# Kernel optimization log

Measured on AMD Instinct MI355X. Metric: run time of the kernel, lower is better.

The kernel has to match this reference:

```python
import jax, jax.numpy as jnp
import numpy as np

IGNORE_INDEX = -100
W_HARD = 0.5
W_SOFT = 0.5
TEMPERATURE = 1.0
BETA = 0.0  # forward KL branch
NORMALIZE_TOPK = True


def setup_inputs() -> dict:
    key = jax.random.key(0)
    ks = jax.random.split(key, 6)
    B, N, D, V, K = 2, 2048, 2048, 32768, 64
    student_input = jax.random.normal(ks[0], (B, N, D), dtype=jnp.float32)
    # scale weight so logits are O(1)-ish and logsumexp is well-behaved in fp32
    student_lm_head_weight = jax.random.normal(ks[1], (V, D), dtype=jnp.float32) * 0.02
    target_token_ids = jax.random.randint(ks[2], (B, N, K), 0, V, dtype=jnp.int64)
    # realistic teacher top-k logprobs: normalized over k
    target_logprobs = jax.nn.log_softmax(jax.random.normal(ks[3], (B, N, K), dtype=jnp.float32), axis=-1)
    target_mask = jax.random.randint(ks[4], (B, N, K), 0, 2, dtype=jnp.int32)
    true_labels = jax.random.randint(ks[5], (B, N), 0, V, dtype=jnp.int64)
    return {
        "student_input": student_input,
        "student_lm_head_weight": student_lm_head_weight,
        "target_token_ids": target_token_ids,
        "target_logprobs": target_logprobs,
        "target_mask": target_mask,
        "true_labels": true_labels,
    }


def reference(student_input, student_lm_head_weight, target_token_ids, target_logprobs, target_mask, true_labels):
    B, N, D = student_input.shape
    K = target_token_ids.shape[-1]
    M = B * N

    x = student_input.reshape(M, D)
    logits = x @ student_lm_head_weight.T  # (M, V)

    # ---- hard CE loss on next-token-shifted labels (sum reduction, ignore_index) ----
    labels = jnp.pad(true_labels, ((0, 0), (0, 1)), constant_values=IGNORE_INDEX)[:, 1:].reshape(M)
    lse_full = jax.nn.logsumexp(logits, axis=-1)  # (M,)
    valid = labels != IGNORE_INDEX
    safe_labels = jnp.where(valid, labels, 0)
    gold = jnp.take_along_axis(logits, safe_labels[:, None], axis=-1)[:, 0]
    ce_loss = jnp.sum(jnp.where(valid, lse_full - gold, 0.0))

    # ---- soft top-k forward-KL loss (beta == 0.0) ----
    s_logits = logits / TEMPERATURE
    s_lse = jax.nn.logsumexp(s_logits, axis=-1, keepdims=True)  # (M, 1)
    tk_ids = target_token_ids.reshape(M, K)
    s_lp_topk = jnp.take_along_axis(s_logits, tk_ids, axis=-1) - s_lse  # (M, K)
    if NORMALIZE_TOPK:
        s_lp_topk = jax.nn.log_softmax(s_lp_topk, axis=-1)
    t_lp = target_logprobs.reshape(M, K)
    mask = target_mask.reshape(M, K).astype(bool)
    fwd_kl = jnp.exp(t_lp) * (t_lp - s_lp_topk)  # per-token forward KL terms
    kd_loss = jnp.sum(jnp.where(mask, fwd_kl, 0.0))
    kd_loss = kd_loss * (TEMPERATURE ** 2)

    return W_SOFT * kd_loss + W_HARD * ce_loss
```

## Files before the change

### kernel.cpp

```cpp
#include <hip/hip_runtime.h>
#include <hip/hip_bf16.h>
#include <stdint.h>

typedef __attribute__((ext_vector_type(4))) float f32x4;

#define D_DIM 2048
#define V_DIM 32768
#define M_DIM 4096
#define N_SEQ 2048
#define K_TOP 64
#define NSLOT 512
#define EBCAP 512
#define WSCALE 64.0f
#define IWSCALE 0.015625f

static __device__ __forceinline__ unsigned int f32_to_e4m3(float x) {
  float ax = fminf(fabsf(x), 448.0f);
  unsigned int s = (__float_as_uint(x) >> 31) << 7;
  if (ax >= 0.015625f) {
    unsigned int m = __float_as_uint(ax);
    unsigned int keep = m >> 20;
    unsigned int rb = (m >> 19) & 1u, st = (m & 0x7FFFFu) != 0u;
    keep += rb & (st | (keep & 1u));
    int v = (int)keep - (120 << 3);
    if (v > 0x7E) v = 0x7E;
    return s | (unsigned int)v;
  } else {
    int m = __float2int_rn(ax * 512.0f);
    return s | (unsigned int)m;
  }
}

typedef __attribute__((address_space(3))) unsigned int lds_u32_t;
typedef const __attribute__((address_space(1))) unsigned int glb_u32_t;
static __device__ __forceinline__ void gload16(const void* g, void* l) {
  __builtin_amdgcn_global_load_lds((glb_u32_t*)g, (lds_u32_t*)l, 16, 0, 0);
}

__global__ void cast_fp8_kernel(const float4* __restrict__ inA, uint2* __restrict__ outA, int nA8,
                                const float4* __restrict__ inB, uint2* __restrict__ outB, int nB8) {
  int i = blockIdx.x * blockDim.x + threadIdx.x;
  int stride = gridDim.x * blockDim.x;
  int tot = nA8 + nB8;
  for (; i < tot; i += stride) {
    const float4* in = (i < nA8) ? inA : inB;
    uint2* out = (i < nA8) ? outA : outB;
    float sc = (i < nA8) ? WSCALE : 1.0f;
    int j = (i < nA8) ? i : i - nA8;
    float4 a = in[2 * j], b = in[2 * j + 1];
    uint2 r;
    r.x = f32_to_e4m3(a.x * sc) | (f32_to_e4m3(a.y * sc) << 8) |
          (f32_to_e4m3(a.z * sc) << 16) | (f32_to_e4m3(a.w * sc) << 24);
    r.y = f32_to_e4m3(b.x * sc) | (f32_to_e4m3(b.y * sc) << 8) |
          (f32_to_e4m3(b.z * sc) << 16) | (f32_to_e4m3(b.w * sc) << 24);
    out[j] = r;
  }
}

__global__ __launch_bounds__(256) void bin_kernel(
    const int* __restrict__ tids, const int* __restrict__ tlab,
    unsigned int* __restrict__ cnt, unsigned int* __restrict__ ebuf) {
  int idx = blockIdx.x * 256 + threadIdx.x;
  if (idx >= M_DIM * (K_TOP + 1)) return;
  int m = idx / (K_TOP + 1), k = idx - m * (K_TOP + 1);
  int id;
  if (k < K_TOP) id = tids[m * K_TOP + k];
  else {
    int n = m & (N_SEQ - 1);
    if (n == N_SEQ - 1) return;
    id = tlab[m + 1];
  }
  int tile = ((m >> 8) << 7) + (id >> 8);
  unsigned int pos = atomicAdd(&cnt[tile], 1u);
  if (pos < EBCAP)
    ebuf[tile * EBCAP + pos] =
        ((unsigned int)k << 16) | ((unsigned int)(m & 255) << 8) | (unsigned int)(id & 255);
}


#define BAR do { __builtin_amdgcn_s_barrier(); asm volatile("" ::: "memory"); } while (0)
#define VMC(N) asm volatile("s_waitcnt vmcnt(" #N ")" ::: "memory")
#define PRIO1 __builtin_amdgcn_s_setprio(1)
#define PRIO0 __builtin_amdgcn_s_setprio(0)

#define LD8(BASE, R, KS) \
  (*(const long*)((BASE) + (R) * 64 + \
     (((2 * (KS) + (kqg >> 1)) ^ ((R) & 3) ^ (((R) >> 2) & 3)) << 4) + ((kqg & 1) << 3)))
#define LDA8(BASE, MI, KS) LD8(BASE, (MI) * 16 + fr, KS)
#define LDB8(BASE, NI, KS) LD8(BASE, brow + (NI) * 16 + fr, KS)

#define STAGE(H) do { \
  int tt_ = (H) >> 2, pos_ = (H) & 3; \
  char* dst_ = ldst + ((tt_ & 1) << 15) + (pos_ << 13); \
  const unsigned char* src_ = ((pos_ & 2) ? aptr : bptr) \
      + ((pos_ & 1) ? (size_t)128 * D_DIM : (size_t)0) + (size_t)tt_ * 64; \
  gload16(src_, dst_); \
} while (0)

#define MFMA_Q(M0, U) do { \
  _Pragma("unroll") \
  for (int ni = 0; ni < 4; ++ni) \
    acc[M0][ni] = __builtin_amdgcn_mfma_f32_16x16x32_fp8_fp8(U[0][0], bfrag[ni][0], acc[M0][ni], 0, 0, 0); \
  _Pragma("unroll") \
  for (int ni = 0; ni < 4; ++ni) \
    acc[(M0) + 1][ni] = __builtin_amdgcn_mfma_f32_16x16x32_fp8_fp8(U[1][0], bfrag[ni][0], acc[(M0) + 1][ni], 0, 0, 0); \
  _Pragma("unroll") \
  for (int ni = 0; ni < 4; ++ni) \
    acc[M0][ni] = __builtin_amdgcn_mfma_f32_16x16x32_fp8_fp8(U[0][1], bfrag[ni][1], acc[M0][ni], 0, 0, 0); \
  _Pragma("unroll") \
  for (int ni = 0; ni < 4; ++ni) \
    acc[(M0) + 1][ni] = __builtin_amdgcn_mfma_f32_16x16x32_fp8_fp8(U[1][1], bfrag[ni][1], acc[(M0) + 1][ni], 0, 0, 0); \
} while (0)

#define TILE1B(T, DOST, NVM, DONEXT) do { \
  char* curA_ = ldsAroot + (((T) & 1) << 15); \
  char* nxtA_ = ldsAroot + ((((T) + 1) & 1) << 15); \
  char* nxtB_ = ldsBroot + ((((T) + 1) & 1) << 15); \
   \
  BAR; \
  if (DOST) STAGE(4 * (T) + 8); \
  PRIO1; MFMA_Q(0, aq); PRIO0; \
  aqn[0][0] = LDA8(curA_, 2, 0); aqn[0][1] = LDA8(curA_, 2, 1); \
  aqn[1][0] = LDA8(curA_, 3, 0); aqn[1][1] = LDA8(curA_, 3, 1); \
   \
  BAR; \
  if (DOST) STAGE(4 * (T) + 9); \
  PRIO1; MFMA_Q(2, aqn); PRIO0; \
  aq[0][0] = LDA8(curA_, 4, 0); aq[0][1] = LDA8(curA_, 4, 1); \
  aq[1][0] = LDA8(curA_, 5, 0); aq[1][1] = LDA8(curA_, 5, 1); \
   \
  BAR; \
  PRIO1; MFMA_Q(4, aq); PRIO0; \
  aqn[0][0] = LDA8(curA_, 6, 0); aqn[0][1] = LDA8(curA_, 6, 1); \
  aqn[1][0] = LDA8(curA_, 7, 0); aqn[1][1] = LDA8(curA_, 7, 1); \
  if ((NVM) == 2) { VMC(2); } else if ((NVM) == 0) { VMC(0); } \
   \
  BAR; \
  if (DOST) { STAGE(4 * (T) + 10); STAGE(4 * (T) + 11); } \
  PRIO1; MFMA_Q(6, aqn); PRIO0; \
  if (DONEXT) { \
    _Pragma("unroll") \
    for (int ni = 0; ni < 4; ++ni) { \
      bfrag[ni][0] = LDB8(nxtB_, ni, 0); bfrag[ni][1] = LDB8(nxtB_, ni, 1); } \
    aq[0][0] = LDA8(nxtA_, 0, 0); aq[0][1] = LDA8(nxtA_, 0, 1); \
    aq[1][0] = LDA8(nxtA_, 1, 0); aq[1][1] = LDA8(nxtA_, 1, 1); \
  } \
} while (0)

__global__ __launch_bounds__(512, 2) void gemm_lse_kernel(
    const unsigned char* __restrict__ x8,
    const unsigned char* __restrict__ w8,
    float* __restrict__ pMax,
    float* __restrict__ pSum,
    const unsigned int* __restrict__ bcnt,
    const unsigned int* __restrict__ ebuf,
    float* __restrict__ gout) {
  __shared__ __align__(16) char lds[131072];

  const int bid0 = blockIdx.x;
  const int mt = (bid0 >> 4) & 15;
  const int vt = ((bid0 >> 8) << 4) | (bid0 & 15);
  const int tid = threadIdx.x, lane = tid & 63, w = tid >> 6;
  const int wr = w >> 2, wc = w & 3;
  const int fr = lane & 15, kqg = lane >> 4;
  const int brow = (wc & 1) * 64;

  const int gcol = (((tid & 3) ^ ((tid >> 2) & 3) ^ ((tid >> 4) & 3)) << 4);
  const unsigned char* aptr = x8 + (size_t)(mt * 256 + (tid >> 2)) * D_DIM + gcol;
  const unsigned char* bptr = w8 + (size_t)(vt * 256 + (tid >> 2)) * D_DIM + gcol;
  char* ldst = lds + tid * 16;

  char* ldsAroot = lds + ((2 + wr) << 13);
  char* ldsBroot = lds + ((wc >> 1) << 13);

  f32x4 acc[8][4];
#pragma unroll
  for (int i = 0; i < 8; i++)
#pragma unroll
    for (int j = 0; j < 4; j++) acc[i][j] = (f32x4){0.f, 0.f, 0.f, 0.f};

  long bfrag[4][2], aq[2][2], aqn[2][2];

  STAGE(0); STAGE(1); STAGE(2); STAGE(3);
  STAGE(4); STAGE(5); STAGE(6); STAGE(7);
  VMC(0);
  BAR;
#pragma unroll
  for (int ni = 0; ni < 4; ++ni) {
    bfrag[ni][0] = LDB8(ldsBroot, ni, 0); bfrag[ni][1] = LDB8(ldsBroot, ni, 1);
  }
  aq[0][0] = LDA8(ldsAroot, 0, 0); aq[0][1] = LDA8(ldsAroot, 0, 1);
  aq[1][0] = LDA8(ldsAroot, 1, 0); aq[1][1] = LDA8(ldsAroot, 1, 1);

  for (int it = 0; it < 15; ++it) {
    TILE1B(2 * it, 1, 2, 1);
    TILE1B(2 * it + 1, 1, 2, 1);
  }
  TILE1B(30, 0, 0, 1);
  TILE1B(31, 0, 99, 0);

  const int slot = vt * 4 + wc;
#pragma unroll
  for (int mi = 0; mi < 8; mi++) {
#pragma unroll
    for (int j = 0; j < 4; j++) {
      const int row = mt * 256 + wr * 128 + mi * 16 + kqg * 4 + j;
      float v0 = acc[mi][0][j] * IWSCALE, v1 = acc[mi][1][j] * IWSCALE;
      float v2 = acc[mi][2][j] * IWSCALE, v3 = acc[mi][3][j] * IWSCALE;
      float mx = fmaxf(fmaxf(v0, v1), fmaxf(v2, v3));
      for (int s = 1; s < 16; s <<= 1) mx = fmaxf(mx, __shfl_xor(mx, s));
      float sm = __expf(v0 - mx) + __expf(v1 - mx) +
                 __expf(v2 - mx) + __expf(v3 - mx);
      for (int s = 1; s < 16; s <<= 1) sm += __shfl_xor(sm, s);
      if (fr == 0) {
        pMax[row * NSLOT + slot] = mx;
        pSum[row * NSLOT + slot] = sm;
      }
    }
  }

  const int tile = (mt << 7) + vt;
  unsigned int cn = bcnt[tile];
  if (cn > EBCAP) cn = EBCAP;
  const unsigned int* elist = ebuf + tile * EBCAP;
  float* ldsf = (float*)lds;

  __syncthreads();
#pragma unroll
  for (int half = 0; half < 2; ++half) {
    if (wr == half) {
#pragma unroll
      for (int mi = 0; mi < 8; mi++) {
        const int r0 = mi * 16 + kqg * 4;
        const int cs = (kqg & 1) << 4;
#pragma unroll
        for (int ni = 0; ni < 4; ni++) {
          const int c0 = (wc * 64 + ni * 16 + fr) ^ cs;
#pragma unroll
          for (int j = 0; j < 4; j++)
            ldsf[(r0 + j) * 256 + c0] = acc[mi][ni][j] * IWSCALE;
        }
      }
    }
    __syncthreads();
    for (unsigned int e = tid; e < cn; e += 512) {
      unsigned int u = elist[e];
      int r = (u >> 8) & 255;
      if ((r >> 7) == half) {
        int c = u & 255, k = u >> 16;
        int rl = r & 127;
        gout[(mt * 256 + r) * (K_TOP + 1) + k] = ldsf[rl * 256 + (c ^ (((rl >> 2) & 1) << 4))];
      }
    }
    __syncthreads();
  }
}

__global__ __launch_bounds__(256) void reduce_kernel(
    const float* __restrict__ pMax, const float* __restrict__ pSum,
    const float* __restrict__ gout, const float* __restrict__ t_lp,
    const int* __restrict__ t_mask, float* __restrict__ out) {
  const int tid = threadIdx.x, lane = tid & 63, w = tid >> 6;
  const int m = blockIdx.x * 4 + w;

  float msl[8], ssl[8];
  float M = -1e30f;
#pragma unroll
  for (int j = 0; j < 8; j++) {
    msl[j] = pMax[m * NSLOT + lane + j * 64];
    ssl[j] = pSum[m * NSLOT + lane + j * 64];
    M = fmaxf(M, msl[j]);
  }
  for (int s = 1; s < 64; s <<= 1) M = fmaxf(M, __shfl_xor(M, s));
  float S = 0.f;
#pragma unroll
  for (int j = 0; j < 8; j++) S += ssl[j] * __expf(msl[j] - M);
  for (int s = 1; s < 64; s <<= 1) S += __shfl_xor(S, s);
  const float lse = M + logf(S);

  const int n = m & (N_SEQ - 1);
  float ce = 0.f;
  if (n < N_SEQ - 1) ce = lse - gout[m * (K_TOP + 1) + K_TOP];

  const float g = gout[m * (K_TOP + 1) + lane];
  float gM = g;
  for (int s = 1; s < 64; s <<= 1) gM = fmaxf(gM, __shfl_xor(gM, s));
  float gE = __expf(g - gM);
  float gS = gE;
  for (int s = 1; s < 64; s <<= 1) gS += __shfl_xor(gS, s);
  const float lseK = gM + logf(gS);

  const float tl = t_lp[m * K_TOP + lane];
  const int mk = t_mask[m * K_TOP + lane];
  float kd = mk ? __expf(tl) * (tl - (g - lseK)) : 0.f;
  for (int s = 1; s < 64; s <<= 1) kd += __shfl_xor(kd, s);

  if (lane == 0) atomicAdd(out, 0.5f * kd + 0.5f * ce);
}

extern "C" void kernel_launch(void* const* d_in, const int* in_sizes, int n_in,
                              void* d_out, int out_size, void* d_ws, size_t ws_size,
                              hipStream_t stream) {
  const float* x   = (const float*)d_in[0];
  const float* Wm  = (const float*)d_in[1];
  const int* tids  = (const int*)d_in[2];
  const float* tlp = (const float*)d_in[3];
  const int* tmask = (const int*)d_in[4];
  const int* tlab  = (const int*)d_in[5];
  float* out = (float*)d_out;

  char* ws = (char*)d_ws;
  unsigned char* w8 = (unsigned char*)ws;
  unsigned char* x8 = (unsigned char*)(ws + (size_t)V_DIM * D_DIM);
  char* p = ws + (size_t)V_DIM * D_DIM + (size_t)M_DIM * D_DIM;
  float* pMax = (float*)p;                       p += (size_t)M_DIM * NSLOT * 4;
  float* pSum = (float*)p;                       p += (size_t)M_DIM * NSLOT * 4;
  float* gout = (float*)p;                       p += (size_t)M_DIM * (K_TOP + 1) * 4;
  unsigned int* bcnt = (unsigned int*)p;         p += 2048 * 4;
  unsigned int* ebuf = (unsigned int*)p;         p += (size_t)2048 * EBCAP * 4;

  hipMemsetAsync(d_out, 0, sizeof(float), stream);
  hipMemsetAsync(bcnt, 0, 2048 * 4, stream);

  bin_kernel<<<(M_DIM * (K_TOP + 1) + 255) / 256, 256, 0, stream>>>(
      tids, tlab, bcnt, ebuf);

  cast_fp8_kernel<<<8192, 256, 0, stream>>>(
      (const float4*)Wm, (uint2*)w8, (V_DIM * D_DIM) / 8,
      (const float4*)x, (uint2*)x8, (M_DIM * D_DIM) / 8);

  gemm_lse_kernel<<<(M_DIM / 256) * (V_DIM / 256), 512, 0, stream>>>(
      x8, w8, pMax, pSum, bcnt, ebuf, gout);

  reduce_kernel<<<M_DIM / 4, 256, 0, stream>>>(pMax, pSum, gout, tlp, tmask, out);
}
```

Measured before the change: 570.2 us.

## Permute fp8 K layout so each lane fetches both MFMA fragments with one 16B LDS read

```diff
diff --git a/kernel.cpp b/kernel.cpp
--- a/kernel.cpp
+++ b/kernel.cpp
@@ -3,6 +3,7 @@
 #include <stdint.h>
 
 typedef __attribute__((ext_vector_type(4))) float f32x4;
+typedef __attribute__((ext_vector_type(2))) long l8x16;
 
 #define D_DIM 2048
 #define V_DIM 32768
@@ -53,7 +54,8 @@
           (f32_to_e4m3(a.z * sc) << 16) | (f32_to_e4m3(a.w * sc) << 24);
     r.y = f32_to_e4m3(b.x * sc) | (f32_to_e4m3(b.y * sc) << 8) |
           (f32_to_e4m3(b.z * sc) << 16) | (f32_to_e4m3(b.w * sc) << 24);
-    out[j] = r;
+    int oj = ((j >> 3) << 3) + ((j & 3) << 1) + ((j >> 2) & 1);
+    out[oj] = r;
   }
 }
 
@@ -83,11 +85,10 @@
 #define PRIO1 __builtin_amdgcn_s_setprio(1)
 #define PRIO0 __builtin_amdgcn_s_setprio(0)
 
-#define LD8(BASE, R, KS) \
-  (*(const long*)((BASE) + (R) * 64 + \
-     (((2 * (KS) + (kqg >> 1)) ^ ((R) & 3) ^ (((R) >> 2) & 3)) << 4) + ((kqg & 1) << 3)))
-#define LDA8(BASE, MI, KS) LD8(BASE, (MI) * 16 + fr, KS)
-#define LDB8(BASE, NI, KS) LD8(BASE, brow + (NI) * 16 + fr, KS)
+#define LDF(BASE, R) \
+  (*(const l8x16*)((BASE) + (R) * 64 + ((kqg ^ (((R) >> 1) & 3)) << 4)))
+#define LDAF(BASE, MI) LDF(BASE, (MI) * 16 + fr)
+#define LDBF(BASE, NI) LDF(BASE, brow + (NI) * 16 + fr)
 
 #define STAGE(H) do { \
   int tt_ = (H) >> 2, pos_ = (H) & 3; \
@@ -97,19 +98,19 @@
   gload16(src_, dst_); \
 } while (0)
 
-#define MFMA_Q(M0, U) do { \
+#define MFMA_Q(M0, U0, U1) do { \
   _Pragma("unroll") \
   for (int ni = 0; ni < 4; ++ni) \
-    acc[M0][ni] = __builtin_amdgcn_mfma_f32_16x16x32_fp8_fp8(U[0][0], bfrag[ni][0], acc[M0][ni], 0, 0, 0); \
+    acc[M0][ni] = __builtin_amdgcn_mfma_f32_16x16x32_fp8_fp8((U0)[0], bF[ni][0], acc[M0][ni], 0, 0, 0); \
   _Pragma("unroll") \
   for (int ni = 0; ni < 4; ++ni) \
-    acc[(M0) + 1][ni] = __builtin_amdgcn_mfma_f32_16x16x32_fp8_fp8(U[1][0], bfrag[ni][0], acc[(M0) + 1][ni], 0, 0, 0); \
+    acc[(M0) + 1][ni] = __builtin_amdgcn_mfma_f32_16x16x32_fp8_fp8((U1)[0], bF[ni][0], acc[(M0) + 1][ni], 0, 0, 0); \
   _Pragma("unroll") \
   for (int ni = 0; ni < 4; ++ni) \
-    acc[M0][ni] = __builtin_amdgcn_mfma_f32_16x16x32_fp8_fp8(U[0][1], bfrag[ni][1], acc[M0][ni], 0, 0, 0); \
+    acc[M0][ni] = __builtin_amdgcn_mfma_f32_16x16x32_fp8_fp8((U0)[1], bF[ni][1], acc[M0][ni], 0, 0, 0); \
   _Pragma("unroll") \
   for (int ni = 0; ni < 4; ++ni) \
-    acc[(M0) + 1][ni] = __builtin_amdgcn_mfma_f32_16x16x32_fp8_fp8(U[1][1], bfrag[ni][1], acc[(M0) + 1][ni], 0, 0, 0); \
+    acc[(M0) + 1][ni] = __builtin_amdgcn_mfma_f32_16x16x32_fp8_fp8((U1)[1], bF[ni][1], acc[(M0) + 1][ni], 0, 0, 0); \
 } while (0)
 
 #define TILE1B(T, DOST, NVM, DONEXT) do { \
@@ -119,31 +120,26 @@
    \
   BAR; \
   if (DOST) STAGE(4 * (T) + 8); \
-  PRIO1; MFMA_Q(0, aq); PRIO0; \
-  aqn[0][0] = LDA8(curA_, 2, 0); aqn[0][1] = LDA8(curA_, 2, 1); \
-  aqn[1][0] = LDA8(curA_, 3, 0); aqn[1][1] = LDA8(curA_, 3, 1); \
+  PRIO1; MFMA_Q(0, a01[0], a01[1]); PRIO0; \
+  a23[0] = LDAF(curA_, 2); a23[1] = LDAF(curA_, 3); \
    \
   BAR; \
   if (DOST) STAGE(4 * (T) + 9); \
-  PRIO1; MFMA_Q(2, aqn); PRIO0; \
-  aq[0][0] = LDA8(curA_, 4, 0); aq[0][1] = LDA8(curA_, 4, 1); \
-  aq[1][0] = LDA8(curA_, 5, 0); aq[1][1] = LDA8(curA_, 5, 1); \
+  PRIO1; MFMA_Q(2, a23[0], a23[1]); PRIO0; \
+  a45[0] = LDAF(curA_, 4); a45[1] = LDAF(curA_, 5); \
    \
   BAR; \
-  PRIO1; MFMA_Q(4, aq); PRIO0; \
-  aqn[0][0] = LDA8(curA_, 6, 0); aqn[0][1] = LDA8(curA_, 6, 1); \
-  aqn[1][0] = LDA8(curA_, 7, 0); aqn[1][1] = LDA8(curA_, 7, 1); \
+  PRIO1; MFMA_Q(4, a45[0], a45[1]); PRIO0; \
+  a67[0] = LDAF(curA_, 6); a67[1] = LDAF(curA_, 7); \
   if ((NVM) == 2) { VMC(2); } else if ((NVM) == 0) { VMC(0); } \
    \
   BAR; \
   if (DOST) { STAGE(4 * (T) + 10); STAGE(4 * (T) + 11); } \
-  PRIO1; MFMA_Q(6, aqn); PRIO0; \
+  PRIO1; MFMA_Q(6, a67[0], a67[1]); PRIO0; \
   if (DONEXT) { \
-    _Pragma("unroll") \
-    for (int ni = 0; ni < 4; ++ni) { \
-      bfrag[ni][0] = LDB8(nxtB_, ni, 0); bfrag[ni][1] = LDB8(nxtB_, ni, 1); } \
-    aq[0][0] = LDA8(nxtA_, 0, 0); aq[0][1] = LDA8(nxtA_, 0, 1); \
-    aq[1][0] = LDA8(nxtA_, 1, 0); aq[1][1] = LDA8(nxtA_, 1, 1); \
+    bF[0] = LDBF(nxtB_, 0); bF[1] = LDBF(nxtB_, 1); \
+    bF[2] = LDBF(nxtB_, 2); bF[3] = LDBF(nxtB_, 3); \
+    a01[0] = LDAF(nxtA_, 0); a01[1] = LDAF(nxtA_, 1); \
   } \
 } while (0)
 
@@ -165,7 +161,7 @@
   const int fr = lane & 15, kqg = lane >> 4;
   const int brow = (wc & 1) * 64;
 
-  const int gcol = (((tid & 3) ^ ((tid >> 2) & 3) ^ ((tid >> 4) & 3)) << 4);
+  const int gcol = (((tid & 3) ^ ((tid >> 3) & 3)) << 4);
   const unsigned char* aptr = x8 + (size_t)(mt * 256 + (tid >> 2)) * D_DIM + gcol;
   const unsigned char* bptr = w8 + (size_t)(vt * 256 + (tid >> 2)) * D_DIM + gcol;
   char* ldst = lds + tid * 16;
@@ -179,18 +175,15 @@
 #pragma unroll
     for (int j = 0; j < 4; j++) acc[i][j] = (f32x4){0.f, 0.f, 0.f, 0.f};
 
-  long bfrag[4][2], aq[2][2], aqn[2][2];
+  l8x16 bF[4], a01[2], a23[2], a45[2], a67[2];
 
   STAGE(0); STAGE(1); STAGE(2); STAGE(3);
   STAGE(4); STAGE(5); STAGE(6); STAGE(7);
   VMC(0);
   BAR;
-#pragma unroll
-  for (int ni = 0; ni < 4; ++ni) {
-    bfrag[ni][0] = LDB8(ldsBroot, ni, 0); bfrag[ni][1] = LDB8(ldsBroot, ni, 1);
-  }
-  aq[0][0] = LDA8(ldsAroot, 0, 0); aq[0][1] = LDA8(ldsAroot, 0, 1);
-  aq[1][0] = LDA8(ldsAroot, 1, 0); aq[1][1] = LDA8(ldsAroot, 1, 1);
+  bF[0] = LDBF(ldsBroot, 0); bF[1] = LDBF(ldsBroot, 1);
+  bF[2] = LDBF(ldsBroot, 2); bF[3] = LDBF(ldsBroot, 3);
+  a01[0] = LDAF(ldsAroot, 0); a01[1] = LDAF(ldsAroot, 1);
 
   for (int it = 0; it < 15; ++it) {
     TILE1B(2 * it, 1, 2, 1);
```

After: 552.2 us. -3.2%, faster.
